# Kernel tuning notes

Hardware: AMD Instinct MI355X
Metric: run time of the kernel (lower is better)

Reference implementation:

```python
import jax, jax.numpy as jnp
import numpy as np

N_Q_HEADS = 32
N_KV_HEADS = 8
D_MODEL = 4096
D_K = 128
D_V = 128
ROPE_BASE = 10000.0


def _rope(x):
    # x: [bs, h, s, d]; llama-style rotate-half RoPE
    d = x.shape[-1]
    s = x.shape[2]
    inv_freq = 1.0 / (ROPE_BASE ** (jnp.arange(0, d, 2, dtype=jnp.float32) / d))  # [d/2]
    ang = jnp.arange(s, dtype=jnp.float32)[:, None] * inv_freq[None, :]  # [s, d/2]
    cos = jnp.concatenate([jnp.cos(ang), jnp.cos(ang)], axis=-1)[None, None]  # [1,1,s,d]
    sin = jnp.concatenate([jnp.sin(ang), jnp.sin(ang)], axis=-1)[None, None]
    x1, x2 = x[..., : d // 2], x[..., d // 2 :]
    rot = jnp.concatenate([-x2, x1], axis=-1)
    return x * cos + rot * sin


def setup_inputs() -> dict:
    key = jax.random.key(0)
    ks = jax.random.split(key, 8)
    bs, s = 2, 1024
    inp = {
        "query": jax.random.normal(ks[0], (bs, s, D_MODEL), dtype=jnp.float32),
        "key": jax.random.normal(ks[1], (bs, s, D_MODEL), dtype=jnp.float32),
        "value": jax.random.normal(ks[2], (bs, s, D_MODEL), dtype=jnp.float32),
        "mask": jnp.ones((bs, s, s), dtype=jnp.float32),
        "wq": jax.random.normal(ks[3], (D_MODEL, N_Q_HEADS * D_K), dtype=jnp.float32) * 0.02,
        "wk": jax.random.normal(ks[4], (D_MODEL, N_KV_HEADS * D_K), dtype=jnp.float32) * 0.02,
        "wv": jax.random.normal(ks[5], (D_MODEL, N_KV_HEADS * D_V), dtype=jnp.float32) * 0.02,
        "wo": jax.random.normal(ks[6], (N_Q_HEADS * D_V, D_MODEL), dtype=jnp.float32) * 0.02,
    }
    return inp


def reference(query, key, value, mask, wq, wk, wv, wo):
    bs, s, _ = query.shape
    g = N_Q_HEADS // N_KV_HEADS  # query heads per kv head

    q = (query @ wq).reshape(bs, s, N_Q_HEADS, D_K).transpose(0, 2, 1, 3)   # [b,Hq,s,dk]
    k = (key @ wk).reshape(bs, s, N_KV_HEADS, D_K).transpose(0, 2, 1, 3)    # [b,Hkv,s,dk]
    v = (value @ wv).reshape(bs, s, N_KV_HEADS, D_V).transpose(0, 2, 1, 3)  # [b,Hkv,s,dv]

    q = _rope(q)
    k = _rope(k)

    scale = jnp.sqrt(jnp.float32(D_K))
    qg = q.reshape(bs, N_KV_HEADS, g, s, D_K)  # group q heads per kv head
    scores = jnp.einsum("bhgqd,bhkd->bhgqk", qg, k) / scale  # [b,Hkv,g,s,s]
    masked = jnp.where(mask[:, None, None].astype(bool), scores, -1e9)
    w = jax.nn.softmax(masked, axis=-1)
    out = jnp.einsum("bhgqk,bhkd->bhgqd", w, v)  # [b,Hkv,g,s,dv]
    out = out.reshape(bs, N_Q_HEADS, s, D_V).transpose(0, 2, 1, 3).reshape(bs, s, N_Q_HEADS * D_V)
    return out @ wo
```

## Files before the change

### kernel.cpp

```cpp
#include <hip/hip_runtime.h>

typedef __attribute__((ext_vector_type(8))) short short8;
typedef __attribute__((ext_vector_type(4))) float f32x4;

__device__ __forceinline__ unsigned short f2bf(float f) {
  unsigned int u = __builtin_bit_cast(unsigned int, f);
  u += 0x7fffu + ((u >> 16) & 1u);
  return (unsigned short)(u >> 16);
}
__device__ __forceinline__ float bf2f(unsigned short h) {
  unsigned int u = ((unsigned int)h) << 16;
  return __builtin_bit_cast(float, u);
}

__device__ __forceinline__ void gld16(const unsigned short* g, unsigned short* l) {
  __builtin_amdgcn_global_load_lds(
      (const __attribute__((address_space(1))) unsigned int*)g,
      (__attribute__((address_space(3))) unsigned int*)l, 16, 0, 0);
}

__global__ __launch_bounds__(256) void cast3_kernel(const float* __restrict__ a, const float* __restrict__ b,
                                                    const float* __restrict__ c, unsigned short* __restrict__ oa,
                                                    unsigned short* __restrict__ ob, unsigned short* __restrict__ oc,
                                                    int n4) {
  int idx = blockIdx.x * 256 + threadIdx.x;
  if (idx >= n4) return;
  const float* in = (blockIdx.y == 0) ? a : (blockIdx.y == 1) ? b : c;
  unsigned short* out = (blockIdx.y == 0) ? oa : (blockIdx.y == 1) ? ob : oc;
  const float4 v = ((const float4*)in)[idx];
  ushort4 o;
  o.x = f2bf(v.x); o.y = f2bf(v.y); o.z = f2bf(v.z); o.w = f2bf(v.w);
  ((ushort4*)out)[idx] = o;
}

__global__ __launch_bounds__(256) void transpose2_kernel(const float* __restrict__ in0, unsigned short* __restrict__ out0,
                                                         const float* __restrict__ in1, unsigned short* __restrict__ out1,
                                                         int K, int N) {
  __shared__ float tile[64][65];
  const float* in = blockIdx.z ? in1 : in0;
  unsigned short* out = blockIdx.z ? out1 : out0;
  const int kb = blockIdx.x * 64, nb = blockIdx.y * 64;
  const int tid = threadIdx.x;
  const int r = tid >> 4;
  const int c = (tid & 15) * 4;
#pragma unroll
  for (int i = 0; i < 4; i++) {
    const float4 v = *(const float4*)(in + (size_t)(kb + r + i * 16) * N + nb + c);
    tile[r + i * 16][c + 0] = v.x;
    tile[r + i * 16][c + 1] = v.y;
    tile[r + i * 16][c + 2] = v.z;
    tile[r + i * 16][c + 3] = v.w;
  }
  __syncthreads();
#pragma unroll
  for (int i = 0; i < 4; i++) {
    int n = r + i * 16;
    ushort4 o;
    o.x = f2bf(tile[c + 0][n]);
    o.y = f2bf(tile[c + 1][n]);
    o.z = f2bf(tile[c + 2][n]);
    o.w = f2bf(tile[c + 3][n]);
    *(ushort4*)(out + (size_t)(nb + n) * K + kb + c) = o;
  }
}

template <int NF, bool F32OUT>
__global__ __launch_bounds__(256, 2) void gemm_lds(const unsigned short* __restrict__ A0,
                                                   const unsigned short* __restrict__ B0, void* __restrict__ C0,
                                                   const unsigned short* __restrict__ A1,
                                                   const unsigned short* __restrict__ B1, void* __restrict__ C1,
                                                   int M, int N, int K) {
  constexpr int TN = NF * 32;
  __shared__ __align__(16) unsigned short As[128 * 64];
  __shared__ __align__(16) unsigned short Bs[TN * 64];
  const unsigned short* A = blockIdx.z ? A1 : A0;
  const unsigned short* BT = blockIdx.z ? B1 : B0;
  void* C = blockIdx.z ? C1 : C0;

  const int m0 = blockIdx.x * 128, n0 = blockIdx.y * TN;
  const int tid = threadIdx.x;
  const int lane = tid & 63;
  const int w = __builtin_amdgcn_readfirstlane(tid >> 6);
  const int wm = (w & 1) * 64, wn = (w >> 1) * (TN / 2);
  const int lr = lane & 15, kg = lane >> 4;
  const int lrow = lane >> 3;
  const int lseg = (lane & 7) ^ lrow;

  const unsigned short* Abase = A + (size_t)(m0 + w * 8 + lrow) * K + lseg * 8;
  const unsigned short* Bbase = BT + (size_t)(n0 + w * 8 + lrow) * K + lseg * 8;

  f32x4 acc[4][NF] = {};
  for (int k0 = 0; k0 < K; k0 += 64) {
#pragma unroll
    for (int i = 0; i < 4; i++)
      gld16(Abase + (size_t)(32 * i) * K + k0, As + (32 * i + w * 8) * 64);
#pragma unroll
    for (int i = 0; i < NF; i++)
      gld16(Bbase + (size_t)(32 * i) * K + k0, Bs + (32 * i + w * 8) * 64);
    __syncthreads();
#pragma unroll
    for (int ks = 0; ks < 2; ks++) {
      short8 af[4], bfg[NF];
#pragma unroll
      for (int mi = 0; mi < 4; mi++) {
        int row = wm + mi * 16 + lr;
        af[mi] = *(const short8*)(As + row * 64 + ((ks * 4 + kg) ^ (lr & 7)) * 8);
      }
#pragma unroll
      for (int ni = 0; ni < NF; ni++) {
        int row = wn + ni * 16 + lr;
        bfg[ni] = *(const short8*)(Bs + row * 64 + ((ks * 4 + kg) ^ (lr & 7)) * 8);
      }
#pragma unroll
      for (int mi = 0; mi < 4; mi++)
#pragma unroll
        for (int ni = 0; ni < NF; ni++)
          acc[mi][ni] = __builtin_amdgcn_mfma_f32_16x16x32_bf16(af[mi], bfg[ni], acc[mi][ni], 0, 0, 0);
    }
    __syncthreads();
  }
#pragma unroll
  for (int mi = 0; mi < 4; mi++)
#pragma unroll
    for (int ni = 0; ni < NF; ni++)
#pragma unroll
      for (int r2 = 0; r2 < 4; r2++) {
        int m = m0 + wm + mi * 16 + kg * 4 + r2;
        int n = n0 + wn + ni * 16 + lr;
        float v = acc[mi][ni][r2];
        if (F32OUT)
          ((float*)C)[(size_t)m * N + n] = v;
        else
          ((unsigned short*)C)[(size_t)m * N + n] = f2bf(v);
      }
}

__global__ __launch_bounds__(256) void rope_kernel(unsigned short* __restrict__ buf, int nheads, int total,
                                                   float oscale) {
  int idx = blockIdx.x * 256 + threadIdx.x;
  if (idx >= total) return;
  int i = idx & 63;
  int h = (idx >> 6) % nheads;
  int row = idx / (64 * nheads);
  int pos = row & 1023;
  float invf = exp2f(-(float)(2 * i) * (13.287712379549449f / 128.f));
  float ang = (float)pos * invf;
  float s, c;
  __sincosf(ang, &s, &c);
  unsigned short* p = buf + (size_t)row * ((size_t)nheads * 128) + h * 128;
  float x1 = bf2f(p[i]), x2 = bf2f(p[i + 64]);
  p[i] = f2bf((x1 * c - x2 * s) * oscale);
  p[i + 64] = f2bf((x2 * c + x1 * s) * oscale);
}

__global__ __launch_bounds__(256) void maskbits_kernel(const float* __restrict__ mask,
                                                       unsigned long long* __restrict__ mb) {
  int idx = blockIdx.x * 256 + threadIdx.x;
  const float4* p = (const float4*)(mask + (size_t)(idx >> 4) * 1024 + (idx & 15) * 64);
  unsigned long long bits = 0ull;
#pragma unroll
  for (int i = 0; i < 16; i++) {
    float4 v = p[i];
    unsigned int g = (unsigned int)(v.x != 0.f) | ((unsigned int)(v.y != 0.f) << 1) |
                     ((unsigned int)(v.z != 0.f) << 2) | ((unsigned int)(v.w != 0.f) << 3);
    bits |= ((unsigned long long)g) << (i * 4);
  }
  mb[idx] = bits;
}

__global__ __launch_bounds__(256, 3) void flash_kernel(const unsigned short* __restrict__ Q,
                                                       const unsigned short* __restrict__ Kbuf,
                                                       const unsigned short* __restrict__ Vbuf,
                                                       const unsigned long long* __restrict__ Mb,
                                                       unsigned short* __restrict__ Ctx) {
  __shared__ unsigned short Vt[2][128][64];
  const int qb = blockIdx.x, h = blockIdx.y, b = blockIdx.z;
  const int hkv = h >> 2;
  const int tid = threadIdx.x, wave = tid >> 6, lane = tid & 63;
  const int lr = lane & 15, kg = lane >> 4;
  const int q0 = qb * 64 + wave * 16;

  auto stageV = [&](int tt) {
    const int k0s = tt * 64;
    unsigned short(*vt)[64] = Vt[tt & 1];
#pragma unroll
    for (int pass = 0; pass < 2; pass++) {
      int kp = (tid >> 4) * 2 + pass * 32;
      int d0 = (tid & 15) * 8;
      short8 v0 = *(const short8*)(Vbuf + (size_t)(b * 1024 + k0s + kp) * 1024 + hkv * 128 + d0);
      short8 v1 = *(const short8*)(Vbuf + (size_t)(b * 1024 + k0s + kp + 1) * 1024 + hkv * 128 + d0);
#pragma unroll
      for (int j = 0; j < 8; j++) {
        int d = d0 + j;
        int kk = kp ^ (((d >> 3) & 7) << 3);
        unsigned int pack = (unsigned int)(unsigned short)v0[j] | ((unsigned int)(unsigned short)v1[j] << 16);
        *(unsigned int*)&vt[d][kk] = pack;
      }
    }
  };

  short8 qf[4];
  {
    const unsigned short* qp = Q + (size_t)(b * 1024 + q0 + lr) * 4096 + h * 128 + kg * 8;
#pragma unroll
    for (int ks = 0; ks < 4; ks++) qf[ks] = *(const short8*)(qp + ks * 32);
  }

  const unsigned short* Kp[4];
#pragma unroll
  for (int nf = 0; nf < 4; nf++) {
    int krow = ((nf & 1) << 5) + ((lr >> 2) << 3) + ((nf >> 1) << 2) + (lr & 3);
    Kp[nf] = Kbuf + (size_t)(b * 1024 + krow) * 1024 + hkv * 128 + kg * 8;
  }
  const unsigned long long* mp = Mb + (size_t)(b * 1024 + q0 + lr) * 16;

  f32x4 o[8] = {};
  float mcur = -1e30f, lcur = 0.f;

  stageV(0);

  for (int t = 0; t < 16; t++) {
    f32x4 s[4] = {};
#pragma unroll
    for (int ks = 0; ks < 4; ks++)
#pragma unroll
      for (int nf = 0; nf < 4; nf++) {
        short8 kf = *(const short8*)(Kp[nf] + (size_t)t * 65536 + ks * 32);
        s[nf] = __builtin_amdgcn_mfma_f32_16x16x32_bf16(kf, qf[ks], s[nf], 0, 0, 0);
      }
    const unsigned long long mbv = mp[t];
    __syncthreads();
    if (t < 15) stageV(t + 1);

    const unsigned int m0b = (unsigned int)(mbv >> (kg * 8)) & 0xffu;
    const unsigned int m1b = (unsigned int)(mbv >> (32 + kg * 8)) & 0xffu;
    float sv[4][4];
#pragma unroll
    for (int nf = 0; nf < 4; nf++) {
      const unsigned int mm = (nf & 1) ? m1b : m0b;
#pragma unroll
      for (int r2 = 0; r2 < 4; r2++) {
        int jj = ((nf >> 1) << 2) + r2;
        sv[nf][r2] = ((mm >> jj) & 1u) ? s[nf][r2] : -1e9f;
      }
    }

    float rmax = sv[0][0];
#pragma unroll
    for (int nf = 0; nf < 4; nf++)
#pragma unroll
      for (int r2 = 0; r2 < 4; r2++) rmax = fmaxf(rmax, sv[nf][r2]);
    rmax = fmaxf(rmax, __shfl_xor(rmax, 16));
    rmax = fmaxf(rmax, __shfl_xor(rmax, 32));

    if (!__all(rmax - mcur <= 8.0f)) {
      float mnew = fmaxf(mcur, rmax);
      float alpha = __expf(mcur - mnew);
      mcur = mnew;
      lcur *= alpha;
      float abc[4];
#pragma unroll
      for (int r2 = 0; r2 < 4; r2++) abc[r2] = __shfl(alpha, kg * 4 + r2);
#pragma unroll
      for (int nf2 = 0; nf2 < 8; nf2++)
#pragma unroll
        for (int r2 = 0; r2 < 4; r2++) o[nf2][r2] *= abc[r2];
    }

    float rsum = 0.f;
    unsigned short pb[4][4];
#pragma unroll
    for (int nf = 0; nf < 4; nf++)
#pragma unroll
      for (int r2 = 0; r2 < 4; r2++) {
        float p = __expf(sv[nf][r2] - mcur);
        rsum += p;
        pb[nf][r2] = f2bf(p);
      }
    rsum += __shfl_xor(rsum, 16);
    rsum += __shfl_xor(rsum, 32);
    lcur += rsum;

    short8 pf[2];
#pragma unroll
    for (int ks2 = 0; ks2 < 2; ks2++) {
      short8 x;
#pragma unroll
      for (int r2 = 0; r2 < 4; r2++) {
        x[r2] = (short)pb[ks2][r2];
        x[4 + r2] = (short)pb[ks2 + 2][r2];
      }
      pf[ks2] = x;
    }

    const unsigned short(*vt)[64] = Vt[t & 1];
#pragma unroll
    for (int ks2 = 0; ks2 < 2; ks2++)
#pragma unroll
      for (int nf2 = 0; nf2 < 8; nf2++) {
        int d = nf2 * 16 + lr;
        int kk = (ks2 * 32 + kg * 8) ^ (((d >> 3) & 7) << 3);
        short8 vf = *(const short8*)&vt[d][kk];
        o[nf2] = __builtin_amdgcn_mfma_f32_16x16x32_bf16(pf[ks2], vf, o[nf2], 0, 0, 0);
      }
  }

  float linv = 1.f / lcur;
  float lbc[4];
#pragma unroll
  for (int r2 = 0; r2 < 4; r2++) lbc[r2] = __shfl(linv, kg * 4 + r2);
#pragma unroll
  for (int nf2 = 0; nf2 < 8; nf2++)
#pragma unroll
    for (int r2 = 0; r2 < 4; r2++) {
      int qq = q0 + kg * 4 + r2;
      int d = nf2 * 16 + lr;
      Ctx[(size_t)(b * 1024 + qq) * 4096 + h * 128 + d] = f2bf(o[nf2][r2] * lbc[r2]);
    }
}

extern "C" void kernel_launch(void* const* d_in, const int* in_sizes, int n_in,
                              void* d_out, int out_size, void* d_ws, size_t ws_size,
                              hipStream_t stream) {
  const float* query = (const float*)d_in[0];
  const float* key   = (const float*)d_in[1];
  const float* value = (const float*)d_in[2];
  const float* mask  = (const float*)d_in[3];
  const float* wq    = (const float*)d_in[4];
  const float* wk    = (const float*)d_in[5];
  const float* wv    = (const float*)d_in[6];
  const float* wo    = (const float*)d_in[7];
  float* out = (float*)d_out;

  char* ws = (char*)d_ws;
  size_t off = 0;
  auto alloc = [&](size_t elems) {
    unsigned short* p = (unsigned short*)(ws + off);
    off += ((elems * 2 + 255) / 256) * 256;
    return p;
  };
  unsigned short* qbf = alloc((size_t)2048 * 4096);
  unsigned short* kbf = alloc((size_t)2048 * 4096);
  unsigned short* vbf = alloc((size_t)2048 * 4096);
  unsigned short* wqT = alloc((size_t)4096 * 4096);
  unsigned short* wkT = alloc((size_t)1024 * 4096);
  unsigned short* wvT = alloc((size_t)1024 * 4096);
  unsigned short* woT = alloc((size_t)4096 * 4096);
  unsigned short* Qb  = alloc((size_t)2048 * 4096);
  unsigned short* Kb  = alloc((size_t)2048 * 1024);
  unsigned short* Vb  = alloc((size_t)2048 * 1024);
  unsigned short* Ctx = qbf;
  unsigned long long* mbits = (unsigned long long*)kbf;

  cast3_kernel<<<dim3(8192, 3), 256, 0, stream>>>(query, key, value, qbf, kbf, vbf, 2048 * 4096 / 4);
  transpose2_kernel<<<dim3(64, 64, 2), 256, 0, stream>>>(wq, wqT, wo, woT, 4096, 4096);
  transpose2_kernel<<<dim3(64, 16, 2), 256, 0, stream>>>(wk, wkT, wv, wvT, 4096, 1024);

  gemm_lds<4, false><<<dim3(16, 32, 1), 256, 0, stream>>>(qbf, wqT, Qb, qbf, wqT, Qb, 2048, 4096, 4096);
  gemm_lds<2, false><<<dim3(16, 16, 2), 256, 0, stream>>>(kbf, wkT, Kb, vbf, wvT, Vb, 2048, 1024, 4096);

  maskbits_kernel<<<128, 256, 0, stream>>>(mask, mbits);

  rope_kernel<<<(2048 * 32 * 64) / 256, 256, 0, stream>>>(Qb, 32, 2048 * 32 * 64, 0.08838834764831845f);
  rope_kernel<<<(2048 * 8 * 64) / 256, 256, 0, stream>>>(Kb, 8, 2048 * 8 * 64, 1.0f);

  flash_kernel<<<dim3(16, 32, 2), 256, 0, stream>>>(Qb, Kb, Vb, mbits, Ctx);

  gemm_lds<4, true><<<dim3(16, 32, 1), 256, 0, stream>>>(Ctx, woT, out, Ctx, woT, out, 2048, 4096, 4096);

  (void)in_sizes; (void)n_in; (void)out_size; (void)ws_size;
}
```

Baseline: 661.6 us.

## Stage K tiles in LDS via async global_load_lds and prefetch V into registers

```diff
diff --git a/kernel.cpp b/kernel.cpp
--- a/kernel.cpp
+++ b/kernel.cpp
@@ -173,27 +173,49 @@
                                                        const unsigned short* __restrict__ Vbuf,
                                                        const unsigned long long* __restrict__ Mb,
                                                        unsigned short* __restrict__ Ctx) {
-  __shared__ unsigned short Vt[2][128][64];
+  __shared__ __align__(16) unsigned short Ks[64 * 128];
+  __shared__ __align__(16) unsigned short Vt[2][128][64];
   const int qb = blockIdx.x, h = blockIdx.y, b = blockIdx.z;
   const int hkv = h >> 2;
   const int tid = threadIdx.x, wave = tid >> 6, lane = tid & 63;
   const int lr = lane & 15, kg = lane >> 4;
   const int q0 = qb * 64 + wave * 16;
 
-  auto stageV = [&](int tt) {
-    const int k0s = tt * 64;
+  const unsigned short* ksrc[4];
+  unsigned short* kdst[4];
+#pragma unroll
+  for (int i = 0; i < 4; i++) {
+    const int rho = 16 * wave + 4 * i + (lane >> 4);
+    const int nf = rho >> 4, l2 = rho & 15;
+    const int grow = ((nf & 1) << 5) + ((l2 >> 2) << 3) + ((nf >> 1) << 2) + (l2 & 3);
+    const int sb = ((((lane & 15) << 4) ^ (l2 << 4)) >> 1);
+    ksrc[i] = Kbuf + (size_t)(b * 1024 + grow) * 1024 + hkv * 128 + sb;
+    kdst[i] = Ks + (16 * wave + 4 * i) * 128;
+  }
+
+  const int vkp = (tid >> 4) * 2;
+  const int vd0 = (tid & 15) * 8;
+  const unsigned short* vsrc = Vbuf + (size_t)(b * 1024) * 1024 + hkv * 128 + vd0;
+  short8 vreg[4];
+  auto loadV = [&](int tt) {
+    const size_t roff = (size_t)(tt * 64) * 1024;
+#pragma unroll
+    for (int p = 0; p < 2; p++) {
+      vreg[2 * p]     = *(const short8*)(vsrc + roff + (size_t)(vkp + p * 32) * 1024);
+      vreg[2 * p + 1] = *(const short8*)(vsrc + roff + (size_t)(vkp + p * 32 + 1) * 1024);
+    }
+  };
+  auto writeV = [&](int tt) {
     unsigned short(*vt)[64] = Vt[tt & 1];
 #pragma unroll
-    for (int pass = 0; pass < 2; pass++) {
-      int kp = (tid >> 4) * 2 + pass * 32;
-      int d0 = (tid & 15) * 8;
-      short8 v0 = *(const short8*)(Vbuf + (size_t)(b * 1024 + k0s + kp) * 1024 + hkv * 128 + d0);
-      short8 v1 = *(const short8*)(Vbuf + (size_t)(b * 1024 + k0s + kp + 1) * 1024 + hkv * 128 + d0);
+    for (int p = 0; p < 2; p++) {
+      const int kp = vkp + p * 32;
 #pragma unroll
       for (int j = 0; j < 8; j++) {
-        int d = d0 + j;
-        int kk = kp ^ (((d >> 3) & 7) << 3);
-        unsigned int pack = (unsigned int)(unsigned short)v0[j] | ((unsigned int)(unsigned short)v1[j] << 16);
+        const int d = vd0 + j;
+        const int kk = kp ^ (((d & 7) ^ ((d >> 3) & 7)) << 3);
+        unsigned int pack = (unsigned int)(unsigned short)vreg[2 * p][j] |
+                            ((unsigned int)(unsigned short)vreg[2 * p + 1][j] << 16);
         *(unsigned int*)&vt[d][kk] = pack;
       }
     }
@@ -205,32 +227,34 @@
 #pragma unroll
     for (int ks = 0; ks < 4; ks++) qf[ks] = *(const short8*)(qp + ks * 32);
   }
-
-  const unsigned short* Kp[4];
-#pragma unroll
-  for (int nf = 0; nf < 4; nf++) {
-    int krow = ((nf & 1) << 5) + ((lr >> 2) << 3) + ((nf >> 1) << 2) + (lr & 3);
-    Kp[nf] = Kbuf + (size_t)(b * 1024 + krow) * 1024 + hkv * 128 + kg * 8;
-  }
   const unsigned long long* mp = Mb + (size_t)(b * 1024 + q0 + lr) * 16;
 
   f32x4 o[8] = {};
   float mcur = -1e30f, lcur = 0.f;
 
-  stageV(0);
+#pragma unroll
+  for (int i = 0; i < 4; i++) gld16(ksrc[i], kdst[i]);
+  loadV(0);
+  writeV(0);
+  __syncthreads();
+
+  const int cswz = lr << 4;
 
   for (int t = 0; t < 16; t++) {
+    if (t < 15) loadV(t + 1);
+
     f32x4 s[4] = {};
+    __builtin_amdgcn_s_setprio(1);
 #pragma unroll
     for (int ks = 0; ks < 4; ks++)
 #pragma unroll
       for (int nf = 0; nf < 4; nf++) {
-        short8 kf = *(const short8*)(Kp[nf] + (size_t)t * 65536 + ks * 32);
+        const int rho = nf * 16 + lr;
+        short8 kf = *(const short8*)(Ks + rho * 128 + (((ks * 64 + kg * 16) ^ cswz) >> 1));
         s[nf] = __builtin_amdgcn_mfma_f32_16x16x32_bf16(kf, qf[ks], s[nf], 0, 0, 0);
       }
+    __builtin_amdgcn_s_setprio(0);
     const unsigned long long mbv = mp[t];
-    __syncthreads();
-    if (t < 15) stageV(t + 1);
 
     const unsigned int m0b = (unsigned int)(mbv >> (kg * 8)) & 0xffu;
     const unsigned int m1b = (unsigned int)(mbv >> (32 + kg * 8)) & 0xffu;
@@ -293,16 +317,26 @@
       pf[ks2] = x;
     }
 
+    __syncthreads();
+    if (t < 15) {
+#pragma unroll
+      for (int i = 0; i < 4; i++) gld16(ksrc[i] + (size_t)(t + 1) * 65536, kdst[i]);
+    }
+
     const unsigned short(*vt)[64] = Vt[t & 1];
+    __builtin_amdgcn_s_setprio(1);
 #pragma unroll
     for (int ks2 = 0; ks2 < 2; ks2++)
 #pragma unroll
       for (int nf2 = 0; nf2 < 8; nf2++) {
         int d = nf2 * 16 + lr;
-        int kk = (ks2 * 32 + kg * 8) ^ (((d >> 3) & 7) << 3);
+        int kk = (ks2 * 32 + kg * 8) ^ (((d & 7) ^ ((d >> 3) & 7)) << 3);
         short8 vf = *(const short8*)&vt[d][kk];
         o[nf2] = __builtin_amdgcn_mfma_f32_16x16x32_bf16(pf[ks2], vf, o[nf2], 0, 0, 0);
       }
+    __builtin_amdgcn_s_setprio(0);
+    if (t < 15) writeV(t + 1);
+    __syncthreads();
   }
 
   float linv = 1.f / lcur;
```

Result: faster. 592.0 us (-10.5%).
